# Kernel tuning notes

Hardware: AMD Instinct MI355X
Metric: run time of the kernel (lower is better)

Reference implementation:

```python
import jax, jax.numpy as jnp
import numpy as np
import math

B = 8192
N_MODELS = 64
T_PER_SPLIT = 16
MAXLEAF = 64
EMB = 32
BN_EPS = 1e-5


def setup_inputs() -> dict:
    key = jax.random.key(0)
    k1, k2, k3 = jax.random.split(key, 3)
    # leaf indices per (sample, model*tree), values in [0, maxleaf)
    x = jax.random.randint(k1, (B, N_MODELS * T_PER_SPLIT), 0, MAXLEAF, dtype=jnp.int32)
    # embed_w ~ N(0, sqrt(1/max_ntree_per_split))
    embed_w = jax.random.normal(k2, (N_MODELS, T_PER_SPLIT * MAXLEAF, EMB), dtype=jnp.float32) * math.sqrt(1.0 / T_PER_SPLIT)
    # BatchNorm1d affine params (gamma=1, beta=0 at init)
    bn_gamma = jnp.ones((N_MODELS * EMB,), dtype=jnp.float32)
    bn_beta = jnp.zeros((N_MODELS * EMB,), dtype=jnp.float32)
    # BatchDense(n_models, embsize, 1): weight (M, E, 1) squeezed to (M, E), bias zeros (M,)
    stdv = math.sqrt(6.0 / (EMB + 1))
    bout_w = jax.random.uniform(k3, (N_MODELS, EMB), dtype=jnp.float32, minval=-stdv, maxval=stdv)
    bout_b = jnp.zeros((N_MODELS,), dtype=jnp.float32)
    return {"x": x, "embed_w": embed_w, "bn_gamma": bn_gamma, "bn_beta": bn_beta,
            "bout_w": bout_w, "bout_b": bout_b}


def reference(x, embed_w, bn_gamma, bn_beta, bout_w, bout_b):
    # x: (B, M*T) int leaf indices; embed_w: (M, T*L, E)
    Bn = x.shape[0]
    M, TL, E = embed_w.shape
    T = x.shape[1] // M
    L = TL // T
    # one_hot + bmm == per-tree gather from embed_w, summed over trees
    idx = x.reshape(Bn, M, T) + jnp.arange(T, dtype=x.dtype) * L  # (B, M, T) into TL axis
    emb = embed_w[jnp.arange(M)[None, :, None], idx]              # (B, M, T, E) gather
    h = emb.sum(axis=2).reshape(Bn, M * E)                        # (B, M*E)
    # BatchNorm1d (training-mode batch statistics, biased variance as in torch)
    mean = h.mean(axis=0)
    var = h.var(axis=0)
    h = (h - mean) / jnp.sqrt(var + BN_EPS) * bn_gamma + bn_beta
    # dropout is identity in eval mode
    h = h.reshape(Bn, M, E)
    # BatchDense: per-model linear E -> 1
    out = jnp.einsum('bme,me->bm', h, bout_w) + bout_b            # (B, M)
    sum_out = out.sum(axis=-1, keepdims=True)                     # (B, 1)
    return (sum_out, out)
```

## Files before the change

kernel.cpp:

```cpp
#include <hip/hip_runtime.h>
#include <hip/hip_fp16.h>

constexpr int B_TOT = 8192;
constexpr int NM    = 64;
constexpr int TT    = 16;
constexpr int LF    = 64;
constexpr int EM    = 32;
constexpr int XROW  = NM * TT;
constexpr int TROWS = TT * LF;

template<int TQ>
__device__ __forceinline__ int4 qbcast(int4 v) {
    constexpr int c = TQ * 0x55;
    int4 r;
    r.x = __builtin_amdgcn_mov_dpp(v.x, c, 0xf, 0xf, true);
    r.y = __builtin_amdgcn_mov_dpp(v.y, c, 0xf, 0xf, true);
    r.z = __builtin_amdgcn_mov_dpp(v.z, c, 0xf, 0xf, true);
    r.w = __builtin_amdgcn_mov_dpp(v.w, c, 0xf, 0xf, true);
    return r;
}

__device__ __forceinline__ __half2 H2(unsigned u) { return *(const __half2*)&u; }

__global__ __launch_bounds__(512, 4) void k_stats_f16(
    const int* __restrict__ x, const float* __restrict__ tbl,
    float* __restrict__ psum, float* __restrict__ psq)
{
    __shared__ uint4 tb[TROWS * 4];
    __shared__ float red[2][8][32];

    const int m     = blockIdx.x & 63;
    const int chunk = blockIdx.x >> 6;
    const int tid   = threadIdx.x;
    const int f     = tid & 3;
    const int grp   = tid >> 2;
    const int b0    = chunk * 1024;

    {
        const float4* __restrict__ src = (const float4*)(tbl + (size_t)m * (TROWS * EM));
#pragma unroll
        for (int i = 0; i < 8; ++i) {
            const int o = tid + i * 512;
            const float4 a = src[o * 2];
            const float4 c = src[o * 2 + 1];
            uint4 p;
            __half2 h0 = __floats2half2_rn(a.x, a.y);
            __half2 h1 = __floats2half2_rn(a.z, a.w);
            __half2 h2 = __floats2half2_rn(c.x, c.y);
            __half2 h3 = __floats2half2_rn(c.z, c.w);
            p.x = *(unsigned*)&h0; p.y = *(unsigned*)&h1;
            p.z = *(unsigned*)&h2; p.w = *(unsigned*)&h3;
            tb[o] = p;
        }
    }

    int4 xr = ((const int4*)(x + (size_t)(b0 + grp) * XROW + m * TT))[f];

    float s[8], s2[8];
#pragma unroll
    for (int k = 0; k < 8; ++k) { s[k] = 0.f; s2[k] = 0.f; }

    __syncthreads();

    for (int p = 0; p < 8; ++p) {
        int4 nxt = xr;
        if (p < 7)
            nxt = ((const int4*)(x + (size_t)(b0 + (p + 1) * 128 + grp) * XROW + m * TT))[f];

        const int4 q0 = qbcast<0>(xr);
        const int4 q1 = qbcast<1>(xr);
        const int4 q2 = qbcast<2>(xr);
        const int4 q3 = qbcast<3>(xr);

        __half2 h0 = __half2(__half(0.f), __half(0.f));
        __half2 h1 = h0, h2 = h0, h3 = h0;

#define GATH(Q, RB)                                                          \
        {                                                                    \
            const uint4 a0 = tb[((Q).x + RB      ) * 4 + f];                 \
            const uint4 a1 = tb[((Q).y + RB +  64) * 4 + f];                 \
            const uint4 a2 = tb[((Q).z + RB + 128) * 4 + f];                 \
            const uint4 a3 = tb[((Q).w + RB + 192) * 4 + f];                 \
            h0 = __hadd2(h0, __hadd2(__hadd2(H2(a0.x), H2(a1.x)),            \
                                     __hadd2(H2(a2.x), H2(a3.x))));          \
            h1 = __hadd2(h1, __hadd2(__hadd2(H2(a0.y), H2(a1.y)),            \
                                     __hadd2(H2(a2.y), H2(a3.y))));          \
            h2 = __hadd2(h2, __hadd2(__hadd2(H2(a0.z), H2(a1.z)),            \
                                     __hadd2(H2(a2.z), H2(a3.z))));          \
            h3 = __hadd2(h3, __hadd2(__hadd2(H2(a0.w), H2(a1.w)),            \
                                     __hadd2(H2(a2.w), H2(a3.w))));          \
        }
        GATH(q0, 0) GATH(q1, 256) GATH(q2, 512) GATH(q3, 768)
#undef GATH

        const __half2 hv[4] = {h0, h1, h2, h3};
#pragma unroll
        for (int k = 0; k < 4; ++k) {
            const float lo = __low2float(hv[k]);
            const float hi = __high2float(hv[k]);
            s[2*k]   += lo;  s2[2*k]   = fmaf(lo, lo, s2[2*k]);
            s[2*k+1] += hi;  s2[2*k+1] = fmaf(hi, hi, s2[2*k+1]);
        }
        xr = nxt;
    }

#pragma unroll
    for (int off = 4; off <= 32; off <<= 1) {
#pragma unroll
        for (int k = 0; k < 8; ++k) {
            s[k]  += __shfl_xor(s[k],  off);
            s2[k] += __shfl_xor(s2[k], off);
        }
    }
    const int wave = tid >> 6;
    if ((tid & 63) < 4) {
#pragma unroll
        for (int k = 0; k < 8; ++k) {
            red[0][wave][f * 8 + k] = s[k];
            red[1][wave][f * 8 + k] = s2[k];
        }
    }
    __syncthreads();
    if (tid < 32) {
        float a = 0.f, a2 = 0.f;
#pragma unroll
        for (int w = 0; w < 8; ++w) { a += red[0][w][tid]; a2 += red[1][w][tid]; }
        psum[(chunk * NM + m) * EM + tid] = a;
        psq [(chunk * NM + m) * EM + tid] = a2;
    }
}

__global__ __launch_bounds__(256) void k_prep(
    const float* __restrict__ tbl,
    const float* __restrict__ gamma, const float* __restrict__ beta,
    const float* __restrict__ bw, const float* __restrict__ bb,
    const float* __restrict__ psum, const float* __restrict__ psq,
    float* __restrict__ Cm, float* __restrict__ g2)
{
    const int m    = blockIdx.x >> 2;
    const int part = blockIdx.x & 3;
    __shared__ float a_s[EM];
    if (threadIdx.x < EM) {
        const int e  = threadIdx.x;
        const int ch = m * EM + e;
        float sum = 0.f, sq = 0.f;
#pragma unroll
        for (int c = 0; c < 8; ++c) {
            sum += psum[(c * NM + m) * EM + e];
            sq  += psq [(c * NM + m) * EM + e];
        }
        const float inv_n = 1.f / (float)B_TOT;
        const float mean = sum * inv_n;
        const float var  = sq * inv_n - mean * mean;
        const float istd = rsqrtf(var + 1e-5f);
        const float g = gamma[ch];
        const float w = bw[ch];
        a_s[e] = istd * g * w;
        float ct = (beta[ch] - mean * istd * g) * w;
#pragma unroll
        for (int off = 16; off > 0; off >>= 1) ct += __shfl_down(ct, off, 32);
        if (e == 0 && part == 0) Cm[m] = bb[m] + ct;
    }
    __syncthreads();

    const float* __restrict__ tblm = tbl + (size_t)m * (TROWS * EM);
    const int row = part * 256 + threadIdx.x;
    const float4* rp = (const float4*)(tblm + row * EM);
    float acc = 0.f;
#pragma unroll
    for (int i = 0; i < 8; ++i) {
        const float4 v = rp[i];
        acc += v.x * a_s[i*4+0] + v.y * a_s[i*4+1]
             + v.z * a_s[i*4+2] + v.w * a_s[i*4+3];
    }
    g2[m * TROWS + row] = acc;
}

__global__ __launch_bounds__(512) void k_out3(
    const int* __restrict__ x, const float* __restrict__ g2,
    const float* __restrict__ Cm, float* __restrict__ out)
{
    __shared__ float g2s[TROWS];
    const int m     = blockIdx.x >> 3;
    const int chunk = blockIdx.x & 7;
    const int tid   = threadIdx.x;
    const int f     = tid & 3;
    const int grp   = tid >> 2;
    const int b0    = chunk * 1024;

    ((float2*)g2s)[tid] = ((const float2*)(g2 + m * TROWS))[tid];

    int4 xq[8];
#pragma unroll
    for (int p = 0; p < 8; ++p)
        xq[p] = ((const int4*)(x + (size_t)(b0 + p * 128 + grp) * XROW + m * TT))[f];

    const float C = Cm[m];
    const int base = f * 256;

    __syncthreads();

#pragma unroll
    for (int p = 0; p < 8; ++p) {
        float d = g2s[base       + xq[p].x]
                + g2s[base +  64 + xq[p].y]
                + g2s[base + 128 + xq[p].z]
                + g2s[base + 192 + xq[p].w];
        d += __shfl_xor(d, 1);
        d += __shfl_xor(d, 2);
        const int b = b0 + p * 128 + grp;
        const float o = d + C;
        if (f == 0) out[B_TOT + (size_t)b * NM + m] = o;
        if (f == 1) atomicAdd(&out[b], o);
    }
}

extern "C" void kernel_launch(void* const* d_in, const int* in_sizes, int n_in,
                              void* d_out, int out_size, void* d_ws, size_t ws_size,
                              hipStream_t stream) {
    const int*   x       = (const int*)d_in[0];
    const float* embed_w = (const float*)d_in[1];
    const float* gamma   = (const float*)d_in[2];
    const float* beta    = (const float*)d_in[3];
    const float* bout_w  = (const float*)d_in[4];
    const float* bout_b  = (const float*)d_in[5];
    float* out = (float*)d_out;

    float* ws   = (float*)d_ws;
    float* psum = ws;
    float* psq  = psum + 16384;
    float* Cm   = psq + 16384;
    float* g2   = Cm + 64;

    k_stats_f16<<<dim3(512), dim3(512), 0, stream>>>(x, embed_w, psum, psq);
    k_prep<<<dim3(256), dim3(256),  0, stream>>>(embed_w, gamma, beta, bout_w,
                                                 bout_b, psum, psq, Cm, g2);
    k_out3<<<dim3(512), dim3(512),  0, stream>>>(x, g2, Cm, out);
}
```

Baseline: 113.1 us.

## Fuse BN prep into output kernel and double batch chunk per stats block

Removes the separate prep kernel. Each output block now folds the batch statistics into per-channel coefficients itself and computes the projected table rows in shared memory. The stats kernel moves to 1024-thread blocks covering 2048 samples, which halves the number of blocks that convert the embedding table to fp16 and the number of partial sums to reduce. In exchange, every output block recomputes the projected table for its model: eight redundant reads per model, served mostly from cache. The stats kernel also runs with fewer, larger blocks.

```diff
diff --git a/kernel.cpp b/kernel.cpp
--- a/kernel.cpp
+++ b/kernel.cpp
@@ -22,25 +22,25 @@
 
 __device__ __forceinline__ __half2 H2(unsigned u) { return *(const __half2*)&u; }
 
-__global__ __launch_bounds__(512, 4) void k_stats_f16(
+__global__ __launch_bounds__(1024, 4) void k_stats4(
     const int* __restrict__ x, const float* __restrict__ tbl,
     float* __restrict__ psum, float* __restrict__ psq)
 {
     __shared__ uint4 tb[TROWS * 4];
-    __shared__ float red[2][8][32];
+    __shared__ float red[2][16][32];
 
     const int m     = blockIdx.x & 63;
     const int chunk = blockIdx.x >> 6;
     const int tid   = threadIdx.x;
     const int f     = tid & 3;
     const int grp   = tid >> 2;
-    const int b0    = chunk * 1024;
+    const int b0    = chunk * 2048;
 
     {
         const float4* __restrict__ src = (const float4*)(tbl + (size_t)m * (TROWS * EM));
 #pragma unroll
-        for (int i = 0; i < 8; ++i) {
-            const int o = tid + i * 512;
+        for (int i = 0; i < 4; ++i) {
+            const int o = tid + i * 1024;
             const float4 a = src[o * 2];
             const float4 c = src[o * 2 + 1];
             uint4 p;
@@ -65,7 +65,7 @@
     for (int p = 0; p < 8; ++p) {
         int4 nxt = xr;
         if (p < 7)
-            nxt = ((const int4*)(x + (size_t)(b0 + (p + 1) * 128 + grp) * XROW + m * TT))[f];
+            nxt = ((const int4*)(x + (size_t)(b0 + (p + 1) * 256 + grp) * XROW + m * TT))[f];
 
         const int4 q0 = qbcast<0>(xr);
         const int4 q1 = qbcast<1>(xr);
@@ -124,63 +124,22 @@
     if (tid < 32) {
         float a = 0.f, a2 = 0.f;
 #pragma unroll
-        for (int w = 0; w < 8; ++w) { a += red[0][w][tid]; a2 += red[1][w][tid]; }
+        for (int w = 0; w < 16; ++w) { a += red[0][w][tid]; a2 += red[1][w][tid]; }
         psum[(chunk * NM + m) * EM + tid] = a;
         psq [(chunk * NM + m) * EM + tid] = a2;
     }
 }
 
-__global__ __launch_bounds__(256) void k_prep(
-    const float* __restrict__ tbl,
+__global__ __launch_bounds__(512) void k_out4(
+    const int* __restrict__ x, const float* __restrict__ tbl,
     const float* __restrict__ gamma, const float* __restrict__ beta,
     const float* __restrict__ bw, const float* __restrict__ bb,
     const float* __restrict__ psum, const float* __restrict__ psq,
-    float* __restrict__ Cm, float* __restrict__ g2)
-{
-    const int m    = blockIdx.x >> 2;
-    const int part = blockIdx.x & 3;
-    __shared__ float a_s[EM];
-    if (threadIdx.x < EM) {
-        const int e  = threadIdx.x;
-        const int ch = m * EM + e;
-        float sum = 0.f, sq = 0.f;
-#pragma unroll
-        for (int c = 0; c < 8; ++c) {
-            sum += psum[(c * NM + m) * EM + e];
-            sq  += psq [(c * NM + m) * EM + e];
-        }
-        const float inv_n = 1.f / (float)B_TOT;
-        const float mean = sum * inv_n;
-        const float var  = sq * inv_n - mean * mean;
-        const float istd = rsqrtf(var + 1e-5f);
-        const float g = gamma[ch];
-        const float w = bw[ch];
-        a_s[e] = istd * g * w;
-        float ct = (beta[ch] - mean * istd * g) * w;
-#pragma unroll
-        for (int off = 16; off > 0; off >>= 1) ct += __shfl_down(ct, off, 32);
-        if (e == 0 && part == 0) Cm[m] = bb[m] + ct;
-    }
-    __syncthreads();
-
-    const float* __restrict__ tblm = tbl + (size_t)m * (TROWS * EM);
-    const int row = part * 256 + threadIdx.x;
-    const float4* rp = (const float4*)(tblm + row * EM);
-    float acc = 0.f;
-#pragma unroll
-    for (int i = 0; i < 8; ++i) {
-        const float4 v = rp[i];
-        acc += v.x * a_s[i*4+0] + v.y * a_s[i*4+1]
-             + v.z * a_s[i*4+2] + v.w * a_s[i*4+3];
-    }
-    g2[m * TROWS + row] = acc;
-}
-
-__global__ __launch_bounds__(512) void k_out3(
-    const int* __restrict__ x, const float* __restrict__ g2,
-    const float* __restrict__ Cm, float* __restrict__ out)
+    float* __restrict__ out)
 {
     __shared__ float g2s[TROWS];
+    __shared__ float a_s[EM + 1];
+
     const int m     = blockIdx.x >> 3;
     const int chunk = blockIdx.x & 7;
     const int tid   = threadIdx.x;
@@ -188,14 +147,53 @@
     const int grp   = tid >> 2;
     const int b0    = chunk * 1024;
 
-    ((float2*)g2s)[tid] = ((const float2*)(g2 + m * TROWS))[tid];
+    if (tid < 32) {
+        const int ch = m * EM + tid;
+        float sum = 0.f, sq = 0.f;
+#pragma unroll
+        for (int c = 0; c < 4; ++c) {
+            sum += psum[(c * NM + m) * EM + tid];
+            sq  += psq [(c * NM + m) * EM + tid];
+        }
+        const float inv_n = 1.f / (float)B_TOT;
+        const float mean  = sum * inv_n;
+        const float var   = sq * inv_n - mean * mean;
+        const float gi    = gamma[ch] * rsqrtf(var + 1e-5f);
+        const float w     = bw[ch];
+        a_s[tid] = gi * w;
+        float ct = (beta[ch] - mean * gi) * w;
+#pragma unroll
+        for (int off = 16; off > 0; off >>= 1) ct += __shfl_down(ct, off, 32);
+        if (tid == 0) a_s[32] = bb[m] + ct;
+    }
 
     int4 xq[8];
 #pragma unroll
     for (int p = 0; p < 8; ++p)
         xq[p] = ((const int4*)(x + (size_t)(b0 + p * 128 + grp) * XROW + m * TT))[f];
 
-    const float C = Cm[m];
+    __syncthreads();
+
+    {
+        const float4* __restrict__ rp =
+            (const float4*)(tbl + (size_t)m * (TROWS * EM)) + tid * 16;
+        float acc0 = 0.f, acc1 = 0.f;
+#pragma unroll
+        for (int i = 0; i < 8; ++i) {
+            const float4 v = rp[i];
+            acc0 += v.x * a_s[i*4+0] + v.y * a_s[i*4+1]
+                  + v.z * a_s[i*4+2] + v.w * a_s[i*4+3];
+        }
+#pragma unroll
+        for (int i = 0; i < 8; ++i) {
+            const float4 v = rp[8 + i];
+            acc1 += v.x * a_s[i*4+0] + v.y * a_s[i*4+1]
+                  + v.z * a_s[i*4+2] + v.w * a_s[i*4+3];
+        }
+        ((float2*)g2s)[tid] = make_float2(acc0, acc1);
+    }
+
+    const float C = a_s[32];
     const int base = f * 256;
 
     __syncthreads();
@@ -228,12 +226,9 @@
 
     float* ws   = (float*)d_ws;
     float* psum = ws;
-    float* psq  = psum + 16384;
-    float* Cm   = psq + 16384;
-    float* g2   = Cm + 64;
-
-    k_stats_f16<<<dim3(512), dim3(512), 0, stream>>>(x, embed_w, psum, psq);
-    k_prep<<<dim3(256), dim3(256),  0, stream>>>(embed_w, gamma, beta, bout_w,
-                                                 bout_b, psum, psq, Cm, g2);
-    k_out3<<<dim3(512), dim3(512),  0, stream>>>(x, g2, Cm, out);
-}
+    float* psq  = psum + 8192;
+
+    k_stats4<<<dim3(256), dim3(1024), 0, stream>>>(x, embed_w, psum, psq);
+    k_out4 <<<dim3(512), dim3(512),  0, stream>>>(x, embed_w, gamma, beta,
+                                                  bout_w, bout_b, psum, psq, out);
+}
```

After: 122.4 us. +8.2%, slower.
